# Kernel optimization log

Measured on AMD Instinct MI355X. Metric: run time of the kernel, lower is better.

Reference implementation:

```python
import jax, jax.numpy as jnp
import numpy as np

N_NODES = 100000
N_EDGES = 1250000
IN_CH = 128
OUT_CH = 64


def setup_inputs() -> dict:
    key = jax.random.key(0)
    k1, k2, k3, k4 = jax.random.split(key, 4)
    x = jax.random.normal(k1, (N_NODES, IN_CH), dtype=jnp.float32)
    edge_index = jax.random.randint(k2, (2, N_EDGES), 0, N_NODES, dtype=jnp.int64)
    edge_weight = jax.random.uniform(k3, (N_EDGES,), dtype=jnp.float32)
    # Xavier-uniform weight, zero bias (as in reset_parameters)
    limit = float(np.sqrt(6.0 / (IN_CH + OUT_CH)))
    W = jax.random.uniform(k4, (IN_CH, OUT_CH), dtype=jnp.float32, minval=-limit, maxval=limit)
    b = jnp.zeros((OUT_CH,), dtype=jnp.float32)
    return {"x": x, "edge_index": edge_index, "edge_weight": edge_weight, "W": W, "b": b}


def reference(x, edge_index, edge_weight, W, b):
    # Dense transform: [N, in] @ [in, out] -> [N, out]
    h = jnp.matmul(x, W)
    row, col = edge_index[0], edge_index[1]
    n = h.shape[0]
    # Weighted in-degree via scatter-add on destination (row)
    deg = jnp.zeros((n,), dtype=h.dtype).at[row].add(edge_weight)
    # deg^-0.5 with inf (deg==0) replaced by 0
    deg_inv_sqrt = jnp.where(deg == 0, jnp.zeros_like(deg), deg ** -0.5)
    norm = deg_inv_sqrt[row] * deg_inv_sqrt[col]  # [E]
    # Gather source features, normalize, scatter-add to destinations
    out = jnp.zeros_like(h).at[row].add(h[col] * norm[:, None])
    return out + b
```

## Files before the change

kernel.cpp:

```cpp
#include <hip/hip_runtime.h>

#define N_NODES 100000
#define N_EDGES 1250000
#define IN_CH 128
#define OUT_CH 64

#define NPB 128
#define ACCS2 33
#define NBINS 782
#define LSTRIDE 783
#define RECCAP 2048
#define NB1 384
#define B1T 512
#define CH1 ((N_EDGES + NB1 - 1) / NB1)
#define MAXU ((CH1 + B1T - 1) / B1T)
#define GEMM_BLOCKS ((N_NODES + 127) / 128)

#define QSCALE 8192.0f
#define QBIAS_F 8388608.0f
#define QBIAS_U 8388608u
#define INV_QSCALE 1.220703125e-4f
#define SCALE_DEG 33554432.0f
#define INV_SCALE_DEG 2.9802322387695312e-08f

typedef __attribute__((ext_vector_type(8))) short short8;
typedef __attribute__((ext_vector_type(4))) float f32x4;

__device__ inline unsigned int f2bf(float f) {
    unsigned int u = __float_as_uint(f);
    unsigned int r = ((u >> 16) & 1u) + 0x7FFFu;
    return (u + r) >> 16;
}
__device__ inline float bf_lo(unsigned int p) { return __uint_as_float(p << 16); }
__device__ inline float bf_hi(unsigned int p) { return __uint_as_float(p & 0xFFFF0000u); }

__device__ inline unsigned long long qpacks(unsigned int p, float sc) {
    unsigned int lo = (unsigned int)__float2int_rn(fmaf(bf_lo(p), sc, QBIAS_F));
    unsigned int hi = (unsigned int)__float2int_rn(fmaf(bf_hi(p), sc, QBIAS_F));
    return ((unsigned long long)hi << 32) | (unsigned long long)lo;
}

__global__ __launch_bounds__(B1T) void sort_kernel(const int* __restrict__ ei,
                                                   const float* __restrict__ ew,
                                                   const float* __restrict__ W,
                                                   unsigned int* __restrict__ Wb,
                                                   int* __restrict__ lscan2d,
                                                   int2* __restrict__ brec) {
    __shared__ int2 srec[CH1];
    __shared__ int shist[NBINS];
    __shared__ int sscan[NBINS + 2];
    __shared__ int ssum[256];
    const int tid = threadIdx.x;

    if (blockIdx.x >= NB1) {
        int g = (blockIdx.x - NB1) * B1T + tid;
        if (g < 1024) {
            int c = g >> 8;
            int t4 = (g >> 6) & 3;
            int l = g & 63;
            int q = l >> 4, r15 = l & 15;
            unsigned int o[4];
#pragma unroll
            for (int jj = 0; jj < 4; ++jj) {
                float f0 = W[(c * 32 + q * 8 + 2 * jj)     * OUT_CH + t4 * 16 + r15];
                float f1 = W[(c * 32 + q * 8 + 2 * jj + 1) * OUT_CH + t4 * 16 + r15];
                o[jj] = f2bf(f0) | (f2bf(f1) << 16);
            }
            *(uint4*)(Wb + (size_t)g * 4) = make_uint4(o[0], o[1], o[2], o[3]);
        }
        return;
    }

    for (int i = tid; i < NBINS; i += B1T) shist[i] = 0;
    __syncthreads();

    const int e0 = blockIdx.x * CH1;
    const int total = (e0 + CH1 < N_EDGES) ? CH1 : N_EDGES - e0;

    int rowv[MAXU], colv[MAXU];
    float wv[MAXU];
#pragma unroll
    for (int u = 0; u < MAXU; ++u) {
        int e = e0 + tid + u * B1T;
        bool ok = (tid + u * B1T) < total;
        rowv[u] = ok ? ei[e] : -1;
        colv[u] = ok ? ei[N_EDGES + e] : 0;
        wv[u]   = ok ? ew[e] : 0.0f;
        if (ok) atomicAdd(&shist[rowv[u] >> 7], 1);
    }
    __syncthreads();

    int a0 = 0, a1 = 0, a2 = 0, a3 = 0, part = 0;
    const int b0 = tid * 4;
    if (tid < 256) {
        a0 = (b0 + 0 < NBINS) ? shist[b0 + 0] : 0;
        a1 = (b0 + 1 < NBINS) ? shist[b0 + 1] : 0;
        a2 = (b0 + 2 < NBINS) ? shist[b0 + 2] : 0;
        a3 = (b0 + 3 < NBINS) ? shist[b0 + 3] : 0;
        part = a0 + a1 + a2 + a3;
        ssum[tid] = part;
    }
    __syncthreads();
#pragma unroll
    for (int d = 1; d < 256; d <<= 1) {
        int add = 0;
        if (tid >= d && tid < 256) add = ssum[tid - d];
        __syncthreads();
        if (tid < 256) ssum[tid] += add;
        __syncthreads();
    }
    if (tid < 256) {
        int base = ssum[tid] - part;
        if (b0 + 0 <= NBINS) sscan[b0 + 0] = base;
        if (b0 + 1 <= NBINS) sscan[b0 + 1] = base + a0;
        if (b0 + 2 <= NBINS) sscan[b0 + 2] = base + a0 + a1;
        if (b0 + 3 <= NBINS) sscan[b0 + 3] = base + a0 + a1 + a2;
    }
    __syncthreads();

    for (int i = tid; i < NBINS; i += B1T) shist[i] = 0;
    __syncthreads();

#pragma unroll
    for (int u = 0; u < MAXU; ++u) {
        if (rowv[u] >= 0) {
            int bb = rowv[u] >> 7;
            int rk = atomicAdd(&shist[bb], 1);
            srec[sscan[bb] + rk] = make_int2(((rowv[u] & 127) << 17) | colv[u],
                                             __float_as_int(wv[u]));
        }
    }
    __syncthreads();

    for (int i = tid; i < total; i += B1T) brec[e0 + i] = srec[i];
    int* lrow = lscan2d + blockIdx.x * LSTRIDE;
    for (int i = tid; i <= NBINS; i += B1T) lrow[i] = sscan[i];
}

__global__ __launch_bounds__(512) void prep_gemm_kernel(const float* __restrict__ x,
                                                        const unsigned int* __restrict__ Wb,
                                                        const int* __restrict__ lscan2d,
                                                        const int2* __restrict__ brec,
                                                        int* __restrict__ brec2,
                                                        float* __restrict__ dis,
                                                        int* __restrict__ qcnt,
                                                        int* __restrict__ mtot,
                                                        unsigned int* __restrict__ hs) {
    __shared__ int sst[NB1];
    __shared__ int segoff[NB1];
    __shared__ int recs[RECCAP];
    __shared__ unsigned long long degcnt[NPB];
    const int tid = threadIdx.x;

    if (blockIdx.x < NBINS) {
        const int b = blockIdx.x;
        if (tid < NPB) degcnt[tid] = 0ull;
        if (tid < NB1) {
            int st = lscan2d[tid * LSTRIDE + b];
            int en = lscan2d[tid * LSTRIDE + b + 1];
            sst[tid] = st;
            segoff[tid] = en - st;
        }
        __syncthreads();
#pragma unroll
        for (int d = 1; d < NB1; d <<= 1) {
            int add = 0;
            if (tid >= d && tid < NB1) add = segoff[tid - d];
            __syncthreads();
            if (tid < NB1) segoff[tid] += add;
            __syncthreads();
        }
        const int m = segoff[NB1 - 1];

        for (int p = tid; p < m; p += 512) {
            int lo = 0, hi = NB1 - 1;
            while (lo < hi) {
                int mid = (lo + hi) >> 1;
                if (segoff[mid] > p) hi = mid; else lo = mid + 1;
            }
            int excl = (lo == 0) ? 0 : segoff[lo - 1];
            int2 rec = brec[(size_t)lo * CH1 + sst[lo] + (p - excl)];
            if (p < RECCAP) recs[p] = rec.x;
            unsigned int qd = (unsigned int)__float2int_rn(__int_as_float(rec.y) * SCALE_DEG);
            atomicAdd(&degcnt[rec.x >> 17], (1ull << 32) | (unsigned long long)qd);
        }
        __syncthreads();

        if (tid < NPB) {
            int node = b * NPB + tid;
            if (node < N_NODES) {
                unsigned long long dc = degcnt[tid];
                float d = (float)(unsigned int)dc * INV_SCALE_DEG;
                dis[node]  = (d == 0.0f) ? 0.0f : (1.0f / sqrtf(d));
                qcnt[node] = (int)(dc >> 32);
            }
        }
        int mc = (m < RECCAP) ? m : RECCAP;
        if (tid == 0) mtot[b] = mc;
        for (int p = tid; p < mc; p += 512)
            brec2[(size_t)b * RECCAP + p] = recs[p];
    } else {
        const int blk  = blockIdx.x - NBINS;
        const int w    = tid >> 6;
        const int lane = tid & 63;
        const int q    = lane >> 4, r15 = lane & 15;
        const int node = blk * 128 + w * 16 + r15;
        const int nl   = (node < N_NODES) ? node : N_NODES - 1;
        const float* xrow = x + (size_t)nl * IN_CH;

        f32x4 acc[4];
#pragma unroll
        for (int t = 0; t < 4; ++t) acc[t] = (f32x4){0.f, 0.f, 0.f, 0.f};

#pragma unroll
        for (int c = 0; c < 4; ++c) {
            float4 xa = *(const float4*)(xrow + c * 32 + q * 8);
            float4 xb = *(const float4*)(xrow + c * 32 + q * 8 + 4);
            short8 bfrag;
            bfrag[0] = (short)f2bf(xa.x); bfrag[1] = (short)f2bf(xa.y);
            bfrag[2] = (short)f2bf(xa.z); bfrag[3] = (short)f2bf(xa.w);
            bfrag[4] = (short)f2bf(xb.x); bfrag[5] = (short)f2bf(xb.y);
            bfrag[6] = (short)f2bf(xb.z); bfrag[7] = (short)f2bf(xb.w);
#pragma unroll
            for (int t = 0; t < 4; ++t) {
                short8 afrag = *(const short8*)(Wb + (size_t)((c * 4 + t) * 64 + lane) * 4);
                acc[t] = __builtin_amdgcn_mfma_f32_16x16x32_bf16(afrag, bfrag, acc[t], 0, 0, 0);
            }
        }

        if (node < N_NODES) {
#pragma unroll
            for (int t = 0; t < 4; ++t) {
                unsigned int p0 = f2bf(acc[t][0]) | (f2bf(acc[t][1]) << 16);
                unsigned int p1 = f2bf(acc[t][2]) | (f2bf(acc[t][3]) << 16);
                *(uint2*)(hs + (size_t)node * 32 + t * 8 + q * 2) = make_uint2(p0, p1);
            }
        }
    }
}

__global__ __launch_bounds__(512) void gather_kernel(const int* __restrict__ mtot,
                                                     const int* __restrict__ brec2,
                                                     const uint4* __restrict__ hs,
                                                     const float* __restrict__ dis,
                                                     const int* __restrict__ qcnt,
                                                     const float* __restrict__ b,
                                                     float* __restrict__ out) {
    __shared__ unsigned long long acc[NPB * ACCS2];
    const int tid = threadIdx.x;
    const int blk = blockIdx.x;
    for (int k = tid; k < NPB * ACCS2; k += 512) acc[k] = 0ull;
    __syncthreads();

    const int m = mtot[blk];
    const int rbase = blk * RECCAP;

    const int wid = tid >> 6, lane = tid & 63;
    const int sub = lane >> 3, l8 = lane & 7;

    for (int j0 = wid * 32; j0 < m; j0 += 256) {
        bool ok[4];
        int rec[4];
        uint4 p[4];
        float sc[4];
#pragma unroll
        for (int s = 0; s < 4; ++s) {
            int jj = j0 + 8 * s + sub;
            ok[s] = jj < m;
            rec[s] = ok[s] ? brec2[rbase + jj] : 0;
        }
#pragma unroll
        for (int s = 0; s < 4; ++s) {
            p[s] = ok[s] ? hs[(size_t)(rec[s] & 0x1FFFF) * 8 + l8]
                         : make_uint4(0, 0, 0, 0);
            sc[s] = ok[s] ? QSCALE * dis[rec[s] & 0x1FFFF] : 0.0f;
        }
#pragma unroll
        for (int s = 0; s < 4; ++s) {
            if (ok[s]) {
                int ba = (rec[s] >> 17) * ACCS2 + 4 * l8;
                atomicAdd(&acc[ba + 0], qpacks(p[s].x, sc[s]));
                atomicAdd(&acc[ba + 1], qpacks(p[s].y, sc[s]));
                atomicAdd(&acc[ba + 2], qpacks(p[s].z, sc[s]));
                atomicAdd(&acc[ba + 3], qpacks(p[s].w, sc[s]));
            }
        }
    }
    __syncthreads();

    const unsigned int* acc32 = (const unsigned int*)acc;
    float bc = b[lane];
    int half = lane & 1, slot = lane >> 1;
#pragma unroll 4
    for (int r = 0; r < 16; ++r) {
        int nl = wid * 16 + r;
        int node = blk * NPB + nl;
        if (node < N_NODES) {
            unsigned int raw = acc32[(nl * ACCS2 + slot) * 2 + half];
            int qsum = (int)(raw - (unsigned int)qcnt[node] * QBIAS_U);
            float di = dis[node] * INV_QSCALE;
            out[(size_t)node * OUT_CH + lane] = (float)qsum * di + bc;
        }
    }
}

extern "C" void kernel_launch(void* const* d_in, const int* in_sizes, int n_in,
                              void* d_out, int out_size, void* d_ws, size_t ws_size,
                              hipStream_t stream) {
    const float* x  = (const float*)d_in[0];
    const int*   ei = (const int*)d_in[1];
    const float* ew = (const float*)d_in[2];
    const float* W  = (const float*)d_in[3];
    const float* b  = (const float*)d_in[4];
    float* out = (float*)d_out;

    unsigned int* hs = (unsigned int*)d_ws;
    unsigned int* Wb = hs + (size_t)N_NODES * 32;
    int* lscan2d = (int*)(Wb + 4096);
    int* mtot    = lscan2d + (size_t)NB1 * LSTRIDE;
    float* dis   = (float*)(mtot + 800);
    int* qcnt    = (int*)(dis + N_NODES);
    int* brec2   = qcnt + N_NODES;
    int2* brec   = (int2*)(brec2 + (size_t)NBINS * RECCAP);
    (void)ws_size; (void)in_sizes; (void)n_in; (void)out_size;

    sort_kernel<<<NB1 + 2, B1T, 0, stream>>>(ei, ew, W, Wb, lscan2d, brec);
    prep_gemm_kernel<<<NBINS + GEMM_BLOCKS, 512, 0, stream>>>(x, Wb, lscan2d, brec,
                                                              brec2, dis, qcnt,
                                                              mtot, hs);
    gather_kernel<<<NBINS, 512, 0, stream>>>(mtot, brec2, (const uint4*)hs,
                                             dis, qcnt, b, out);
}
```

Baseline: 159.2 us.

## Drop compacted record buffer; gather reads sorted segments directly

```diff
diff --git a/kernel.cpp b/kernel.cpp
--- a/kernel.cpp
+++ b/kernel.cpp
@@ -9,7 +9,6 @@
 #define ACCS2 33
 #define NBINS 782
 #define LSTRIDE 783
-#define RECCAP 2048
 #define NB1 384
 #define B1T 512
 #define CH1 ((N_EDGES + NB1 - 1) / NB1)
@@ -137,70 +136,17 @@
     for (int i = tid; i <= NBINS; i += B1T) lrow[i] = sscan[i];
 }
 
-__global__ __launch_bounds__(512) void prep_gemm_kernel(const float* __restrict__ x,
-                                                        const unsigned int* __restrict__ Wb,
-                                                        const int* __restrict__ lscan2d,
-                                                        const int2* __restrict__ brec,
-                                                        int* __restrict__ brec2,
-                                                        float* __restrict__ dis,
-                                                        int* __restrict__ qcnt,
-                                                        int* __restrict__ mtot,
-                                                        unsigned int* __restrict__ hs) {
-    __shared__ int sst[NB1];
-    __shared__ int segoff[NB1];
-    __shared__ int recs[RECCAP];
-    __shared__ unsigned long long degcnt[NPB];
+__global__ __launch_bounds__(512) void deg_gemm_kernel(const float* __restrict__ x,
+                                                       const unsigned int* __restrict__ Wb,
+                                                       const int* __restrict__ lscan2d,
+                                                       const int2* __restrict__ brec,
+                                                       float* __restrict__ dis,
+                                                       int* __restrict__ qcnt,
+                                                       unsigned int* __restrict__ hs) {
     const int tid = threadIdx.x;
 
-    if (blockIdx.x < NBINS) {
-        const int b = blockIdx.x;
-        if (tid < NPB) degcnt[tid] = 0ull;
-        if (tid < NB1) {
-            int st = lscan2d[tid * LSTRIDE + b];
-            int en = lscan2d[tid * LSTRIDE + b + 1];
-            sst[tid] = st;
-            segoff[tid] = en - st;
-        }
-        __syncthreads();
-#pragma unroll
-        for (int d = 1; d < NB1; d <<= 1) {
-            int add = 0;
-            if (tid >= d && tid < NB1) add = segoff[tid - d];
-            __syncthreads();
-            if (tid < NB1) segoff[tid] += add;
-            __syncthreads();
-        }
-        const int m = segoff[NB1 - 1];
-
-        for (int p = tid; p < m; p += 512) {
-            int lo = 0, hi = NB1 - 1;
-            while (lo < hi) {
-                int mid = (lo + hi) >> 1;
-                if (segoff[mid] > p) hi = mid; else lo = mid + 1;
-            }
-            int excl = (lo == 0) ? 0 : segoff[lo - 1];
-            int2 rec = brec[(size_t)lo * CH1 + sst[lo] + (p - excl)];
-            if (p < RECCAP) recs[p] = rec.x;
-            unsigned int qd = (unsigned int)__float2int_rn(__int_as_float(rec.y) * SCALE_DEG);
-            atomicAdd(&degcnt[rec.x >> 17], (1ull << 32) | (unsigned long long)qd);
-        }
-        __syncthreads();
-
-        if (tid < NPB) {
-            int node = b * NPB + tid;
-            if (node < N_NODES) {
-                unsigned long long dc = degcnt[tid];
-                float d = (float)(unsigned int)dc * INV_SCALE_DEG;
-                dis[node]  = (d == 0.0f) ? 0.0f : (1.0f / sqrtf(d));
-                qcnt[node] = (int)(dc >> 32);
-            }
-        }
-        int mc = (m < RECCAP) ? m : RECCAP;
-        if (tid == 0) mtot[b] = mc;
-        for (int p = tid; p < mc; p += 512)
-            brec2[(size_t)b * RECCAP + p] = recs[p];
-    } else {
-        const int blk  = blockIdx.x - NBINS;
+    if (blockIdx.x < GEMM_BLOCKS) {
+        const int blk  = blockIdx.x;
         const int w    = tid >> 6;
         const int lane = tid & 63;
         const int q    = lane >> 4, r15 = lane & 15;
@@ -236,53 +182,112 @@
                 *(uint2*)(hs + (size_t)node * 32 + t * 8 + q * 2) = make_uint2(p0, p1);
             }
         }
-    }
-}
-
-__global__ __launch_bounds__(512) void gather_kernel(const int* __restrict__ mtot,
-                                                     const int* __restrict__ brec2,
+    } else {
+        __shared__ unsigned long long degcnt[NPB];
+        const int b = blockIdx.x - GEMM_BLOCKS;
+        if (tid < NPB) degcnt[tid] = 0ull;
+        __syncthreads();
+        if (tid < NB1) {
+            int st = lscan2d[tid * LSTRIDE + b];
+            int en = lscan2d[tid * LSTRIDE + b + 1];
+            const int2* seg = brec + (size_t)tid * CH1;
+            for (int j = st; j < en; ++j) {
+                int2 r = seg[j];
+                unsigned int qd = (unsigned int)__float2int_rn(__int_as_float(r.y) * SCALE_DEG);
+                atomicAdd(&degcnt[r.x >> 17], (1ull << 32) | (unsigned long long)qd);
+            }
+        }
+        __syncthreads();
+        if (tid < NPB) {
+            int node = b * NPB + tid;
+            if (node < N_NODES) {
+                unsigned long long dc = degcnt[tid];
+                float d = (float)(unsigned int)dc * INV_SCALE_DEG;
+                dis[node]  = (d == 0.0f) ? 0.0f : (1.0f / sqrtf(d));
+                qcnt[node] = (int)(dc >> 32);
+            }
+        }
+    }
+}
+
+__global__ __launch_bounds__(512) void gather_kernel(const int* __restrict__ lscan2d,
+                                                     const int2* __restrict__ brec,
                                                      const uint4* __restrict__ hs,
                                                      const float* __restrict__ dis,
                                                      const int* __restrict__ qcnt,
                                                      const float* __restrict__ b,
                                                      float* __restrict__ out) {
     __shared__ unsigned long long acc[NPB * ACCS2];
+    __shared__ int sst[NB1];
+    __shared__ int soff[NB1];
     const int tid = threadIdx.x;
     const int blk = blockIdx.x;
     for (int k = tid; k < NPB * ACCS2; k += 512) acc[k] = 0ull;
-    __syncthreads();
-
-    const int m = mtot[blk];
-    const int rbase = blk * RECCAP;
+    if (tid < NB1) {
+        int st = lscan2d[tid * LSTRIDE + blk];
+        int en = lscan2d[tid * LSTRIDE + blk + 1];
+        sst[tid]  = st;
+        soff[tid] = en - st;
+    }
+    __syncthreads();
+#pragma unroll
+    for (int d = 1; d < NB1; d <<= 1) {
+        int add = 0;
+        if (tid >= d && tid < NB1) add = soff[tid - d];
+        __syncthreads();
+        if (tid < NB1) soff[tid] += add;
+        __syncthreads();
+    }
+    const int m = soff[NB1 - 1];
 
     const int wid = tid >> 6, lane = tid & 63;
-    const int sub = lane >> 3, l8 = lane & 7;
-
-    for (int j0 = wid * 32; j0 < m; j0 += 256) {
+    const int grp = wid * 8 + (lane >> 3);
+    const int l8  = lane & 7;
+    const int per = (m + 63) >> 6;
+    const int p0  = grp * per;
+    const int p1  = (p0 + per < m) ? p0 + per : m;
+
+    int lo = 0;
+    if (p0 < m) {
+        int hi = NB1 - 1;
+        while (lo < hi) {
+            int mid = (lo + hi) >> 1;
+            if (soff[mid] > p0) hi = mid; else lo = mid + 1;
+        }
+    }
+    int excl = (lo == 0) ? 0 : soff[lo - 1];
+
+    for (int p = p0; p < p1; p += 4) {
         bool ok[4];
         int rec[4];
-        uint4 p[4];
+        uint4 hv[4];
         float sc[4];
+        int plo = lo, pexcl = excl;
 #pragma unroll
         for (int s = 0; s < 4; ++s) {
-            int jj = j0 + 8 * s + sub;
-            ok[s] = jj < m;
-            rec[s] = ok[s] ? brec2[rbase + jj] : 0;
-        }
+            int pp = p + s;
+            ok[s] = pp < p1;
+            rec[s] = 0;
+            if (ok[s]) {
+                while (pp >= soff[plo]) { pexcl = soff[plo]; ++plo; }
+                rec[s] = brec[(size_t)plo * CH1 + sst[plo] + (pp - pexcl)].x;
+            }
+        }
+        lo = plo; excl = pexcl;
 #pragma unroll
         for (int s = 0; s < 4; ++s) {
-            p[s] = ok[s] ? hs[(size_t)(rec[s] & 0x1FFFF) * 8 + l8]
-                         : make_uint4(0, 0, 0, 0);
+            hv[s] = ok[s] ? hs[(size_t)(rec[s] & 0x1FFFF) * 8 + l8]
+                          : make_uint4(0, 0, 0, 0);
             sc[s] = ok[s] ? QSCALE * dis[rec[s] & 0x1FFFF] : 0.0f;
         }
 #pragma unroll
         for (int s = 0; s < 4; ++s) {
             if (ok[s]) {
                 int ba = (rec[s] >> 17) * ACCS2 + 4 * l8;
-                atomicAdd(&acc[ba + 0], qpacks(p[s].x, sc[s]));
-                atomicAdd(&acc[ba + 1], qpacks(p[s].y, sc[s]));
-                atomicAdd(&acc[ba + 2], qpacks(p[s].z, sc[s]));
-                atomicAdd(&acc[ba + 3], qpacks(p[s].w, sc[s]));
+                atomicAdd(&acc[ba + 0], qpacks(hv[s].x, sc[s]));
+                atomicAdd(&acc[ba + 1], qpacks(hv[s].y, sc[s]));
+                atomicAdd(&acc[ba + 2], qpacks(hv[s].z, sc[s]));
+                atomicAdd(&acc[ba + 3], qpacks(hv[s].w, sc[s]));
             }
         }
     }
@@ -317,17 +322,14 @@
     unsigned int* hs = (unsigned int*)d_ws;
     unsigned int* Wb = hs + (size_t)N_NODES * 32;
     int* lscan2d = (int*)(Wb + 4096);
-    int* mtot    = lscan2d + (size_t)NB1 * LSTRIDE;
-    float* dis   = (float*)(mtot + 800);
+    float* dis   = (float*)(lscan2d + (size_t)NB1 * LSTRIDE);
     int* qcnt    = (int*)(dis + N_NODES);
-    int* brec2   = qcnt + N_NODES;
-    int2* brec   = (int2*)(brec2 + (size_t)NBINS * RECCAP);
+    int2* brec   = (int2*)(qcnt + N_NODES);
     (void)ws_size; (void)in_sizes; (void)n_in; (void)out_size;
 
     sort_kernel<<<NB1 + 2, B1T, 0, stream>>>(ei, ew, W, Wb, lscan2d, brec);
-    prep_gemm_kernel<<<NBINS + GEMM_BLOCKS, 512, 0, stream>>>(x, Wb, lscan2d, brec,
-                                                              brec2, dis, qcnt,
-                                                              mtot, hs);
-    gather_kernel<<<NBINS, 512, 0, stream>>>(mtot, brec2, (const uint4*)hs,
+    deg_gemm_kernel<<<GEMM_BLOCKS + NBINS, 512, 0, stream>>>(x, Wb, lscan2d, brec,
+                                                             dis, qcnt, hs);
+    gather_kernel<<<NBINS, 512, 0, stream>>>(lscan2d, brec, (const uint4*)hs,
                                              dis, qcnt, b, out);
 }
```

Result: slower. 168.3 us (+5.7%).
